# Kernel tuning notes

Hardware: AMD Instinct MI355X
Metric: run time of the kernel (lower is better)

## Reference

```python
import jax, jax.numpy as jnp
import numpy as np

N = 100000      # nodes (single node type)
E = 800000      # edges per relation
R = 3           # relations
IN = 128        # in_dim
HID = 32        # hidden_dim per head
H1 = 4          # heads in conv1
OUT = 128       # out_dim (1 head in conv2)
NEG_SLOPE = 0.2 # DGL GATConv default leaky_relu slope


def setup_inputs() -> dict:
    key = jax.random.key(0)
    ks = jax.random.split(key, 10)
    s = 0.05
    x = jax.random.normal(ks[0], (N, IN), dtype=jnp.float32)
    edge_src = jax.random.randint(ks[1], (R, E), 0, N, dtype=jnp.int32)
    edge_dst = jax.random.randint(ks[2], (R, E), 0, N, dtype=jnp.int32)
    # conv1: per-relation GATConv(IN -> HID, 4 heads)
    W1 = jax.random.normal(ks[3], (R, IN, H1 * HID), dtype=jnp.float32) * s
    b1 = jnp.zeros((R, H1 * HID), dtype=jnp.float32)
    al1 = jax.random.normal(ks[4], (R, H1, HID), dtype=jnp.float32) * s
    ar1 = jax.random.normal(ks[5], (R, H1, HID), dtype=jnp.float32) * s
    # conv2: per-relation GATConv(H1*HID -> OUT, 1 head)
    W2 = jax.random.normal(ks[6], (R, H1 * HID, OUT), dtype=jnp.float32) * s
    b2 = jnp.zeros((R, OUT), dtype=jnp.float32)
    al2 = jax.random.normal(ks[7], (R, 1, OUT), dtype=jnp.float32) * s
    ar2 = jax.random.normal(ks[8], (R, 1, OUT), dtype=jnp.float32) * s
    return {"x": x, "edge_src": edge_src, "edge_dst": edge_dst,
            "W1": W1, "b1": b1, "al1": al1, "ar1": ar1,
            "W2": W2, "b2": b2, "al2": al2, "ar2": ar2}


def _gat_rel(h, src, dst, W, b, al, ar):
    """One DGL GATConv (eval mode) on one relation. h: [N, F_in]; al/ar: [H, D]."""
    Hh, D = al.shape
    feat = (h @ W).reshape(N, Hh, D)                 # [N, H, D]
    el = jnp.sum(feat * al, axis=-1)                 # [N, H]
    er = jnp.sum(feat * ar, axis=-1)                 # [N, H]
    e = jax.nn.leaky_relu(el[src] + er[dst], NEG_SLOPE)   # [E, H]
    # edge softmax over incoming edges of each dst node
    m = jax.lax.stop_gradient(jax.ops.segment_max(e, dst, num_segments=N))
    ex = jnp.exp(e - m[dst])
    denom = jax.ops.segment_sum(ex, dst, num_segments=N)  # [N, H]
    a = ex / jnp.maximum(denom[dst], 1e-9)                # [E, H]
    msg = a[:, :, None] * feat[src]                       # [E, H, D]
    rst = jax.ops.segment_sum(msg, dst, num_segments=N)   # [N, H, D]
    # residual: in_feats == H*D so res_fc is Identity; plus bias
    return rst + h.reshape(N, Hh, D) + b.reshape(Hh, D)


def reference(x, edge_src, edge_dst, W1, b1, al1, ar1, W2, b2, al2, ar2):
    # conv1: HeteroGraphConv mean over relations
    h1 = jnp.zeros((N, H1, HID), dtype=x.dtype)
    for r in range(R):
        h1 = h1 + _gat_rel(x, edge_src[r], edge_dst[r], W1[r], b1[r], al1[r], ar1[r])
    h1 = h1 / R
    h = jax.nn.elu(h1.reshape(N, H1 * HID))  # flatten(1) + ELU (dropout = eval no-op)
    # conv2: mean over relations, 1 head
    h2 = jnp.zeros((N, 1, OUT), dtype=x.dtype)
    for r in range(R):
        h2 = h2 + _gat_rel(h, edge_src[r], edge_dst[r], W2[r], b2[r], al2[r], ar2[r])
    h2 = h2 / R
    return h2.reshape(N, OUT)  # squeeze(1)
```

## Files before the change

kernel.cpp:

```cpp
#include <hip/hip_runtime.h>
#include <hip/hip_bf16.h>

#define NN 100000
#define NE 800000
#define NR 3
#define F 128
#define M3 (NR * NN)
#define E3 (NR * NE)
#define NB1 ((M3 + 255) / 256)
#define NPASS 2
#define PW ((NN + NPASS - 1) / NPASS)
#define BPM (36 * 512)

typedef __bf16 bf16x8 __attribute__((ext_vector_type(8)));
typedef float f32x4 __attribute__((ext_vector_type(4)));
typedef float f32x2 __attribute__((ext_vector_type(2)));

__device__ __forceinline__ float lrelu(float v) { return v >= 0.f ? v : 0.2f * v; }
__device__ __forceinline__ unsigned short f2bf(float f) {
    __hip_bfloat16 h = __float2bfloat16(f);
    unsigned short u;
    __builtin_memcpy(&u, &h, 2);
    return u;
}
__device__ __forceinline__ f32x2 fp8x2_to_f32(unsigned short u) {
    return __builtin_amdgcn_cvt_pk_f32_fp8((int)u, false);
}
__device__ __forceinline__ unsigned pack4_fp8(float a, float b, float c, float d) {
    unsigned lo = __builtin_amdgcn_cvt_pk_fp8_f32(a, b, 0, false);
    return __builtin_amdgcn_cvt_pk_fp8_f32(c, d, lo, true);
}

__device__ __forceinline__ void hist_body(int i, const int* __restrict__ edst,
                                          int* __restrict__ counts,
                                          int* __restrict__ eoff) {
    if (i >= E3) return;
    int r = i / NE;
    eoff[i] = atomicAdd(&counts[r * NN + edst[i]], 1);
}

__device__ __forceinline__ void scatter_body(int i, int lo, const int* __restrict__ esrc,
                                             const int* __restrict__ edst,
                                             const int* __restrict__ row_ptr,
                                             const int* __restrict__ eoff,
                                             int* __restrict__ csr_src) {
    if (i >= E3) return;
    int d = edst[i];
    if (d < lo || d >= lo + PW) return;
    int r = i / NE;
    csr_src[row_ptr[r * NN + d] + eoff[i]] = esrc[i];
}

__device__ __forceinline__ void packW_body(int idx, const float* __restrict__ W1,
                                           const float* __restrict__ W2,
                                           const float* __restrict__ al1,
                                           const float* __restrict__ ar1,
                                           const float* __restrict__ al2,
                                           const float* __restrict__ ar2,
                                           unsigned short* __restrict__ Bp) {
    if (idx >= 6 * BPM) return;
    int j = idx & 7;
    int l = (idx >> 3) & 63;
    int tile = (idx >> 9) % 36;
    int m = idx / BPM;
    int ct = tile >> 2, kk = tile & 3;
    int k = kk * 32 + (l >> 4) * 8 + j;
    const float* W = (m < 3) ? (W1 + (size_t)m * (F * F)) : (W2 + (size_t)(m - 3) * (F * F));
    float v = 0.f;
    if (ct < 8) {
        int col = ct * 16 + (l & 15);
        v = W[k * F + col];
    } else {
        int cc = l & 15;
        int Hm = (m < 3) ? 4 : 1;
        int Dm = F / Hm;
        const float* alm = (m < 3) ? (al1 + m * F) : (al2 + (m - 3) * F);
        const float* arm = (m < 3) ? (ar1 + m * F) : (ar2 + (m - 3) * F);
        if (cc < Hm) {
            for (int d = 0; d < Dm; ++d) v += W[k * F + cc * Dm + d] * alm[cc * Dm + d];
        } else if (cc >= 4 && cc < 4 + Hm) {
            int h = cc - 4;
            for (int d = 0; d < Dm; ++d) v += W[k * F + h * Dm + d] * arm[h * Dm + d];
        }
    }
    Bp[idx] = f2bf(v);
}

template <int H>
__device__ __forceinline__ void gemm_body(int bx, int t, const float* __restrict__ A,
                                          const unsigned short* __restrict__ Bp,
                                          unsigned char* __restrict__ Y,
                                          float* __restrict__ el,
                                          float* __restrict__ er) {
    __shared__ __align__(16) unsigned short alds[128 * 128];
    const int row0 = bx * 128;
#pragma unroll
    for (int it = 0; it < 16; ++it) {
        int g = it * 256 + t;
        int row = g >> 5, k4 = g & 31;
        int gr = row0 + row;
        float4 v;
        if (gr < NN) v = *(const float4*)(A + (size_t)gr * F + k4 * 4);
        else v = make_float4(0.f, 0.f, 0.f, 0.f);
        unsigned int lo = (unsigned)f2bf(v.x) | ((unsigned)f2bf(v.y) << 16);
        unsigned int hi = (unsigned)f2bf(v.z) | ((unsigned)f2bf(v.w) << 16);
        int k2 = k4 * 8;
        int byte = row * 256 + ((k2 & ~15) ^ ((row & 7) << 4)) + (k2 & 15);
        *(uint2*)((char*)alds + byte) = make_uint2(lo, hi);
    }
    __syncthreads();

    const int wv = t >> 6, lane = t & 63;
    const int lr = lane & 15;
    const int lkq = lane >> 4;
    for (int m = 0; m < NR; ++m) {
        const bf16x8* bp = (const bf16x8*)(Bp + (size_t)m * BPM);
        f32x4 acc[2][8];
        f32x4 accE[2];
#pragma unroll
        for (int rt = 0; rt < 2; ++rt) {
            accE[rt] = (f32x4){0.f, 0.f, 0.f, 0.f};
#pragma unroll
            for (int ct = 0; ct < 8; ++ct) acc[rt][ct] = (f32x4){0.f, 0.f, 0.f, 0.f};
        }
#pragma unroll
        for (int kk = 0; kk < 4; ++kk) {
            bf16x8 afr[2];
#pragma unroll
            for (int rt = 0; rt < 2; ++rt) {
                int row = wv * 32 + rt * 16 + lr;
                int k2 = kk * 64 + lkq * 16;
                int byte = row * 256 + (k2 ^ ((row & 7) << 4));
                afr[rt] = *(const bf16x8*)((const char*)alds + byte);
            }
#pragma unroll
            for (int ct = 0; ct < 8; ++ct) {
                bf16x8 b = bp[(ct * 4 + kk) * 64 + lane];
                acc[0][ct] = __builtin_amdgcn_mfma_f32_16x16x32_bf16(b, afr[0], acc[0][ct], 0, 0, 0);
                acc[1][ct] = __builtin_amdgcn_mfma_f32_16x16x32_bf16(b, afr[1], acc[1][ct], 0, 0, 0);
            }
            bf16x8 bE = bp[(32 + kk) * 64 + lane];
            accE[0] = __builtin_amdgcn_mfma_f32_16x16x32_bf16(bE, afr[0], accE[0], 0, 0, 0);
            accE[1] = __builtin_amdgcn_mfma_f32_16x16x32_bf16(bE, afr[1], accE[1], 0, 0, 0);
        }
        unsigned char* Yp = Y + (size_t)m * NN * F;
        float* elp = el + (size_t)m * NN * H;
        float* erp = er + (size_t)m * NN * H;
#pragma unroll
        for (int rt = 0; rt < 2; ++rt) {
            int n = row0 + wv * 32 + rt * 16 + lr;
            if (n < NN) {
                size_t rb = (size_t)n * F;
#pragma unroll
                for (int ct = 0; ct < 8; ++ct) {
                    unsigned pk = pack4_fp8(acc[rt][ct][0], acc[rt][ct][1],
                                            acc[rt][ct][2], acc[rt][ct][3]);
                    *(unsigned*)(Yp + rb + ct * 16 + lkq * 4) = pk;
                }
                if (H == 4) {
                    if (lkq == 0)
                        *(float4*)&elp[(size_t)n * 4] = make_float4(accE[rt][0], accE[rt][1],
                                                                    accE[rt][2], accE[rt][3]);
                    else if (lkq == 1)
                        *(float4*)&erp[(size_t)n * 4] = make_float4(accE[rt][0], accE[rt][1],
                                                                    accE[rt][2], accE[rt][3]);
                } else {
                    if (lkq == 0) elp[n] = accE[rt][0];
                    else if (lkq == 1) erp[n] = accE[rt][0];
                }
            }
        }
    }
}

__global__ __launch_bounds__(256) void packw_hist_kernel(const float* __restrict__ W1,
                                                         const float* __restrict__ W2,
                                                         const float* __restrict__ al1,
                                                         const float* __restrict__ ar1,
                                                         const float* __restrict__ al2,
                                                         const float* __restrict__ ar2,
                                                         unsigned short* __restrict__ Bp,
                                                         const int* __restrict__ edst,
                                                         int* __restrict__ counts,
                                                         int* __restrict__ eoff,
                                                         int pw_grid) {
    if ((int)blockIdx.x < pw_grid)
        packW_body(blockIdx.x * 256 + threadIdx.x, W1, W2, al1, ar1, al2, ar2, Bp);
    else
        hist_body((blockIdx.x - pw_grid) * 256 + threadIdx.x, edst, counts, eoff);
}

template <int H>
__global__ __launch_bounds__(256) void gemm_scatter_kernel(const float* __restrict__ A,
                                                           const unsigned short* __restrict__ Bp,
                                                           unsigned char* __restrict__ Y,
                                                           float* __restrict__ el,
                                                           float* __restrict__ er,
                                                           const int* __restrict__ esrc,
                                                           const int* __restrict__ edst,
                                                           const int* __restrict__ row_ptr,
                                                           const int* __restrict__ eoff,
                                                           int* __restrict__ csr_src,
                                                           int gemm_grid, int eg3) {
    if ((int)blockIdx.x < gemm_grid) {
        gemm_body<H>(blockIdx.x, threadIdx.x, A, Bp, Y, el, er);
    } else {
        int b = blockIdx.x - gemm_grid;
        int pass = b / eg3;
        int i = (b - pass * eg3) * 256 + threadIdx.x;
        scatter_body(i, pass * PW, esrc, edst, row_ptr, eoff, csr_src);
    }
}

__global__ __launch_bounds__(256) void scan1_kernel(int* __restrict__ data,
                                                    int* __restrict__ bsum, int n) {
    __shared__ int lds[256];
    int i = blockIdx.x * 256 + threadIdx.x;
    int v = (i < n) ? data[i] : 0;
    lds[threadIdx.x] = v;
    __syncthreads();
#pragma unroll
    for (int off = 1; off < 256; off <<= 1) {
        int t = (threadIdx.x >= off) ? lds[threadIdx.x - off] : 0;
        __syncthreads();
        lds[threadIdx.x] += t;
        __syncthreads();
    }
    int incl = lds[threadIdx.x];
    if (i < n) data[i] = incl - v;
    if (threadIdx.x == 255) bsum[blockIdx.x] = incl;
}

__global__ __launch_bounds__(256) void scan2_kernel(int* __restrict__ bsum, int nb) {
    __shared__ int lds[256];
    int carry = 0;
    for (int base = 0; base < nb; base += 256) {
        int i = base + threadIdx.x;
        int v = (i < nb) ? bsum[i] : 0;
        lds[threadIdx.x] = v;
        __syncthreads();
#pragma unroll
        for (int off = 1; off < 256; off <<= 1) {
            int t = (threadIdx.x >= off) ? lds[threadIdx.x - off] : 0;
            __syncthreads();
            lds[threadIdx.x] += t;
            __syncthreads();
        }
        if (i < nb) bsum[i] = (lds[threadIdx.x] - v) + carry;
        int tot = lds[255];
        __syncthreads();
        carry += tot;
    }
}

__global__ __launch_bounds__(256) void scan3_kernel(int* __restrict__ row_ptr,
                                                    const int* __restrict__ bsum, int n) {
    int i = blockIdx.x * 256 + threadIdx.x;
    if (i >= n) return;
    row_ptr[i] += bsum[blockIdx.x];
}

template <int H, int FIN>
__global__ __launch_bounds__(256) void aggr3_kernel(const int* __restrict__ row_ptr,
                                                    const int* __restrict__ csr_src,
                                                    const float* __restrict__ el,
                                                    const float* __restrict__ er,
                                                    const unsigned char* __restrict__ featb,
                                                    const float* __restrict__ resid,
                                                    const float* __restrict__ bias,
                                                    float* __restrict__ outp) {
    const int gid = blockIdx.x * 256 + threadIdx.x;
    const int d = gid >> 6;
    const int lane = gid & 63;
    if (d >= NN) return;
    const int half = lane >> 5;
    const int fi = (lane & 31) * 4;
    const int CH = (H == 4) ? 16 : 64;
    const int myh = (H == 4) ? (fi >> 5) : 0;
    const int ph = (H == 4) ? (lane >> 4) : 0;
    const int sub = lane & (CH - 1);
    const int grpbase = (H == 4) ? myh * 16 : 0;
    float a0 = 0.f, a1 = 0.f, a2 = 0.f, a3 = 0.f;
    for (int r = 0; r < NR; ++r) {
        const int idx = r * NN + d;
        const int rs = row_ptr[idx];
        const int re = (idx + 1 < M3) ? row_ptr[idx + 1] : E3;
        const float erh = er[(size_t)r * NN * H + d * H + ph];
        const float* elr = el + (size_t)r * NN * H;
        const unsigned char* fb = featb + (size_t)r * NN * F;
        float den = 0.f, b0 = 0.f, b1 = 0.f, b2 = 0.f, b3 = 0.f;
        for (int base = rs; base < re; base += CH) {
            int cnt = re - base;
            if (cnt > CH) cnt = CH;
            int s_l = 0;
            float w_l = 0.f;
            if (sub < cnt) {
                s_l = csr_src[base + sub];
                w_l = __expf(lrelu(elr[s_l * H + ph] + erh));
            }
            den += w_l;
            for (int j = 0; j < cnt; j += 8) {
                int sj[4];
                float wj[4];
#pragma unroll
                for (int q = 0; q < 4; ++q) {
                    int e = j + 2 * q + half;
                    int ec = e < cnt ? e : cnt - 1;
                    sj[q] = __shfl(s_l, grpbase + ec);
                    float w = __shfl(w_l, grpbase + ec);
                    wj[q] = (e < cnt) ? w : 0.f;
                }
                unsigned u[4];
#pragma unroll
                for (int q = 0; q < 4; ++q)
                    u[q] = *(const unsigned*)(fb + (size_t)sj[q] * F + fi);
#pragma unroll
                for (int q = 0; q < 4; ++q) {
                    f32x2 d0 = fp8x2_to_f32((unsigned short)(u[q] & 0xffff));
                    f32x2 d1 = fp8x2_to_f32((unsigned short)(u[q] >> 16));
                    b0 += wj[q] * d0.x;
                    b1 += wj[q] * d0.y;
                    b2 += wj[q] * d1.x;
                    b3 += wj[q] * d1.y;
                }
            }
        }
#pragma unroll
        for (int off = CH >> 1; off; off >>= 1) den += __shfl_xor(den, off);
        float dh = (H == 4) ? __shfl(den, grpbase) : den;
        float rd = 1.f / fmaxf(dh, 1e-9f);
        a0 += b0 * rd;
        a1 += b1 * rd;
        a2 += b2 * rd;
        a3 += b3 * rd;
    }
    a0 += __shfl_xor(a0, 32);
    a1 += __shfl_xor(a1, 32);
    a2 += __shfl_xor(a2, 32);
    a3 += __shfl_xor(a3, 32);
    if (half == 0) {
        const float third = 1.f / 3.f;
        size_t o = (size_t)d * F + fi;
        float4 bA = *(const float4*)&bias[fi];
        float4 bB = *(const float4*)&bias[F + fi];
        float4 bC = *(const float4*)&bias[2 * F + fi];
        float4 rv = *(const float4*)&resid[o];
        float v0 = a0 * third + rv.x + (bA.x + bB.x + bC.x) * third;
        float v1 = a1 * third + rv.y + (bA.y + bB.y + bC.y) * third;
        float v2 = a2 * third + rv.z + (bA.z + bB.z + bC.z) * third;
        float v3 = a3 * third + rv.w + (bA.w + bB.w + bC.w) * third;
        if (FIN == 1) {
            v0 = v0 > 0.f ? v0 : (__expf(v0) - 1.f);
            v1 = v1 > 0.f ? v1 : (__expf(v1) - 1.f);
            v2 = v2 > 0.f ? v2 : (__expf(v2) - 1.f);
            v3 = v3 > 0.f ? v3 : (__expf(v3) - 1.f);
        }
        *(float4*)&outp[o] = make_float4(v0, v1, v2, v3);
    }
}

extern "C" void kernel_launch(void* const* d_in, const int* in_sizes, int n_in,
                              void* d_out, int out_size, void* d_ws, size_t ws_size,
                              hipStream_t stream) {
    const float* x   = (const float*)d_in[0];
    const int* esrc  = (const int*)d_in[1];
    const int* edst  = (const int*)d_in[2];
    const float* W1  = (const float*)d_in[3];
    const float* b1  = (const float*)d_in[4];
    const float* al1 = (const float*)d_in[5];
    const float* ar1 = (const float*)d_in[6];
    const float* W2  = (const float*)d_in[7];
    const float* b2  = (const float*)d_in[8];
    const float* al2 = (const float*)d_in[9];
    const float* ar2 = (const float*)d_in[10];
    float* out = (float*)d_out;

    char* p = (char*)d_ws;
    unsigned char* featb = (unsigned char*)p;    p += (size_t)NR * NN * F;
    float* el    = (float*)p;                    p += (size_t)NR * NN * 4 * 4;
    float* er    = (float*)p;                    p += (size_t)NR * NN * 4 * 4;
    int* row_ptr = (int*)p;                      p += (size_t)M3 * 4;
    int* bsum    = (int*)p;                      p += (size_t)((NB1 + 63) & ~63) * 4;
    int* csr_src = (int*)p;                      p += (size_t)E3 * 4;
    int* eoff    = (int*)p;                      p += (size_t)E3 * 4;
    unsigned short* Bpack = (unsigned short*)p;  p += (size_t)6 * BPM * 2;
    float* h1 = out;

    dim3 b256(256);
    const int eg3 = (E3 + 255) / 256;
    const int gemm_grid = (NN + 127) / 128;
    const int agg = (NN * 64 + 255) / 256;
    const int pw_grid = (6 * BPM + 255) / 256;

    hipMemsetAsync(row_ptr, 0, (size_t)M3 * 4, stream);
    packw_hist_kernel<<<pw_grid + eg3, b256, 0, stream>>>(W1, W2, al1, ar1, al2, ar2, Bpack,
                                                          edst, row_ptr, eoff, pw_grid);
    scan1_kernel<<<NB1, b256, 0, stream>>>(row_ptr, bsum, M3);
    scan2_kernel<<<1, b256, 0, stream>>>(bsum, NB1);
    scan3_kernel<<<NB1, b256, 0, stream>>>(row_ptr, bsum, M3);

    gemm_scatter_kernel<4><<<gemm_grid + NPASS * eg3, b256, 0, stream>>>(
        x, Bpack, featb, el, er, esrc, edst, row_ptr, eoff, csr_src, gemm_grid, eg3);

    aggr3_kernel<4, 1><<<agg, b256, 0, stream>>>(row_ptr, csr_src, el, er, featb, x, b1, h1);

    gemm_scatter_kernel<1><<<gemm_grid, b256, 0, stream>>>(
        h1, Bpack + (size_t)3 * BPM, featb, el, er, esrc, edst, row_ptr, eoff, csr_src,
        gemm_grid, eg3);

    aggr3_kernel<1, 2><<<agg, b256, 0, stream>>>(row_ptr, csr_src, el, er, featb, h1, b2, out);
}
```

Measured before the change: 490.0 us.

## Halve GEMM row tile and stage fp8 output through LDS for coalesced stores

The feature GEMM tile shrinks from 128 to 64 rows per block, so each wave handles one 16-row tile and the grid doubles. The fp8-packed results now go into a padded LDS buffer first and are then written to global memory as 16-byte coalesced stores, instead of scattered 4-byte stores. The intent is better write coalescing and more blocks in flight. The cost is extra LDS traffic, two more barriers per relation, and each B fragment being reused over half as many rows.

```diff
diff --git a/kernel.cpp b/kernel.cpp
--- a/kernel.cpp
+++ b/kernel.cpp
@@ -11,6 +11,7 @@
 #define NPASS 2
 #define PW ((NN + NPASS - 1) / NPASS)
 #define BPM (36 * 512)
+#define GR 64
 
 typedef __bf16 bf16x8 __attribute__((ext_vector_type(8)));
 typedef float f32x4 __attribute__((ext_vector_type(4)));
@@ -92,10 +93,11 @@
                                           unsigned char* __restrict__ Y,
                                           float* __restrict__ el,
                                           float* __restrict__ er) {
-    __shared__ __align__(16) unsigned short alds[128 * 128];
-    const int row0 = bx * 128;
-#pragma unroll
-    for (int it = 0; it < 16; ++it) {
+    __shared__ __align__(16) unsigned short alds[GR * 128];
+    __shared__ __align__(16) unsigned char olds[GR * 144];
+    const int row0 = bx * GR;
+#pragma unroll
+    for (int it = 0; it < 8; ++it) {
         int g = it * 256 + t;
         int row = g >> 5, k4 = g & 31;
         int gr = row0 + row;
@@ -113,63 +115,57 @@
     const int wv = t >> 6, lane = t & 63;
     const int lr = lane & 15;
     const int lkq = lane >> 4;
+    const int n = row0 + wv * 16 + lr;
     for (int m = 0; m < NR; ++m) {
         const bf16x8* bp = (const bf16x8*)(Bp + (size_t)m * BPM);
-        f32x4 acc[2][8];
-        f32x4 accE[2];
-#pragma unroll
-        for (int rt = 0; rt < 2; ++rt) {
-            accE[rt] = (f32x4){0.f, 0.f, 0.f, 0.f};
-#pragma unroll
-            for (int ct = 0; ct < 8; ++ct) acc[rt][ct] = (f32x4){0.f, 0.f, 0.f, 0.f};
-        }
+        f32x4 acc[8];
+        f32x4 accE = (f32x4){0.f, 0.f, 0.f, 0.f};
+#pragma unroll
+        for (int ct = 0; ct < 8; ++ct) acc[ct] = (f32x4){0.f, 0.f, 0.f, 0.f};
 #pragma unroll
         for (int kk = 0; kk < 4; ++kk) {
-            bf16x8 afr[2];
-#pragma unroll
-            for (int rt = 0; rt < 2; ++rt) {
-                int row = wv * 32 + rt * 16 + lr;
-                int k2 = kk * 64 + lkq * 16;
-                int byte = row * 256 + (k2 ^ ((row & 7) << 4));
-                afr[rt] = *(const bf16x8*)((const char*)alds + byte);
-            }
+            int row = wv * 16 + lr;
+            int k2 = kk * 64 + lkq * 16;
+            int byte = row * 256 + (k2 ^ ((row & 7) << 4));
+            bf16x8 afr = *(const bf16x8*)((const char*)alds + byte);
 #pragma unroll
             for (int ct = 0; ct < 8; ++ct) {
                 bf16x8 b = bp[(ct * 4 + kk) * 64 + lane];
-                acc[0][ct] = __builtin_amdgcn_mfma_f32_16x16x32_bf16(b, afr[0], acc[0][ct], 0, 0, 0);
-                acc[1][ct] = __builtin_amdgcn_mfma_f32_16x16x32_bf16(b, afr[1], acc[1][ct], 0, 0, 0);
+                acc[ct] = __builtin_amdgcn_mfma_f32_16x16x32_bf16(b, afr, acc[ct], 0, 0, 0);
             }
             bf16x8 bE = bp[(32 + kk) * 64 + lane];
-            accE[0] = __builtin_amdgcn_mfma_f32_16x16x32_bf16(bE, afr[0], accE[0], 0, 0, 0);
-            accE[1] = __builtin_amdgcn_mfma_f32_16x16x32_bf16(bE, afr[1], accE[1], 0, 0, 0);
-        }
+            accE = __builtin_amdgcn_mfma_f32_16x16x32_bf16(bE, afr, accE, 0, 0, 0);
+        }
+#pragma unroll
+        for (int ct = 0; ct < 8; ++ct) {
+            unsigned pk = pack4_fp8(acc[ct][0], acc[ct][1], acc[ct][2], acc[ct][3]);
+            *(unsigned*)(olds + (wv * 16 + lr) * 144 + ct * 16 + lkq * 4) = pk;
+        }
+        __syncthreads();
         unsigned char* Yp = Y + (size_t)m * NN * F;
+#pragma unroll
+        for (int it2 = 0; it2 < 2; ++it2) {
+            int c = it2 * 256 + t;
+            int row = c >> 3, cc = c & 7;
+            int gr = row0 + row;
+            if (gr < NN)
+                *(uint4*)(Yp + (size_t)gr * F + cc * 16) =
+                    *(const uint4*)(olds + row * 144 + cc * 16);
+        }
         float* elp = el + (size_t)m * NN * H;
         float* erp = er + (size_t)m * NN * H;
-#pragma unroll
-        for (int rt = 0; rt < 2; ++rt) {
-            int n = row0 + wv * 32 + rt * 16 + lr;
-            if (n < NN) {
-                size_t rb = (size_t)n * F;
-#pragma unroll
-                for (int ct = 0; ct < 8; ++ct) {
-                    unsigned pk = pack4_fp8(acc[rt][ct][0], acc[rt][ct][1],
-                                            acc[rt][ct][2], acc[rt][ct][3]);
-                    *(unsigned*)(Yp + rb + ct * 16 + lkq * 4) = pk;
-                }
-                if (H == 4) {
-                    if (lkq == 0)
-                        *(float4*)&elp[(size_t)n * 4] = make_float4(accE[rt][0], accE[rt][1],
-                                                                    accE[rt][2], accE[rt][3]);
-                    else if (lkq == 1)
-                        *(float4*)&erp[(size_t)n * 4] = make_float4(accE[rt][0], accE[rt][1],
-                                                                    accE[rt][2], accE[rt][3]);
-                } else {
-                    if (lkq == 0) elp[n] = accE[rt][0];
-                    else if (lkq == 1) erp[n] = accE[rt][0];
-                }
+        if (n < NN) {
+            if (H == 4) {
+                if (lkq == 0)
+                    *(float4*)&elp[(size_t)n * 4] = make_float4(accE[0], accE[1], accE[2], accE[3]);
+                else if (lkq == 1)
+                    *(float4*)&erp[(size_t)n * 4] = make_float4(accE[0], accE[1], accE[2], accE[3]);
+            } else {
+                if (lkq == 0) elp[n] = accE[0];
+                else if (lkq == 1) erp[n] = accE[0];
             }
         }
+        __syncthreads();
     }
 }
 
@@ -388,7 +384,7 @@
 
     dim3 b256(256);
     const int eg3 = (E3 + 255) / 256;
-    const int gemm_grid = (NN + 127) / 128;
+    const int gemm_grid = (NN + GR - 1) / GR;
     const int agg = (NN * 64 + 255) / 256;
     const int pw_grid = (6 * BPM + 255) / 256;
 
```

After: 441.1 us (median of 2 runs). -10.0%, faster.
